# Optimization experiments

Hardware: AMD Instinct MI355X
Metric: run time of the kernel (lower is better)

The kernel has to match this reference:

```python
import jax, jax.numpy as jnp
import numpy as np

K_CHEB = 3  # Chebyshev order K -> K+1 basis matrices, gcn order = K


def setup_inputs() -> dict:
    key = jax.random.key(0)
    ks = jax.random.split(key, 7)
    B, N, T, Cin, Cout, ndim = 32, 512, 12, 64, 64, 40
    support_len = K_CHEB + 1
    cin_total = (K_CHEB * support_len + 1) * Cin  # (order*support_len+1)*c_in = 832
    x = jax.random.normal(ks[0], (B, N, T, Cin), jnp.float32)
    adj = (jax.random.uniform(ks[1], (N, N)) < 0.05).astype(jnp.float32)
    adjacency = jnp.maximum(adj, jnp.eye(N, dtype=jnp.float32))
    embedding = jax.random.uniform(ks[2], (N, ndim), dtype=jnp.float32)  # nn.init.uniform_
    W1 = jax.random.normal(ks[3], (ndim, ndim // 2), jnp.float32) * 0.3
    W2 = jax.random.normal(ks[4], (ndim, ndim // 2), jnp.float32) * 0.3
    mlp_w = jax.random.normal(ks[5], (Cout, cin_total), jnp.float32) / np.float32(np.sqrt(cin_total))
    mlp_b = jnp.zeros((Cout,), jnp.float32)
    return {"x": x, "adjacency": adjacency, "embedding": embedding,
            "W1": W1, "W2": W2, "mlp_w": mlp_w, "mlp_b": mlp_b}


def _cheb_kernels(adjacency, embedding, W1, W2):
    # adaptive adjacency: embedding mixed through column-softmaxed projections
    e1 = embedding @ jax.nn.softmax(W1, axis=0)
    e2 = embedding @ jax.nn.softmax(W2, axis=0)
    e1 = e1 / (jnp.linalg.norm(e1, axis=1, keepdims=True) + 1e-8)
    e2 = e2 / (jnp.linalg.norm(e2, axis=1, keepdims=True) + 1e-8)
    weight = e1 @ e2.T  # (N, N)
    A = jnp.where(adjacency > 0.0, weight + adjacency, jnp.asarray(9e-15, adjacency.dtype))
    # symmetric normalization: L = I - D^-1/2 A D^-1/2 ; Ls = (2/maxeig)*L - I with maxeig=2 -> Ls = -sym(A)
    d = 1.0 / jnp.sqrt(A.sum(axis=1))
    Ls = -(d[:, None] * A * d[None, :])
    I = jnp.eye(A.shape[0], dtype=A.dtype)
    kernels = [I, Ls]
    for _ in range(1, K_CHEB):  # Chebyshev recursion: T_{k+1} = 2 Ls T_k - T_{k-1}
        kernels.append(2.0 * (Ls @ kernels[-1]) - kernels[-2])
    return kernels  # K_CHEB + 1 matrices of (N, N)


def reference(x, adjacency, embedding, W1, W2, mlp_w, mlp_b):
    supports = _cheb_kernels(adjacency, embedding, W1, W2)
    xp = jnp.transpose(x, (0, 3, 1, 2))  # (B, Cin, N, T)
    out = [xp]
    for a in supports:
        x1 = jnp.einsum('bcvt,vw->bcwt', xp, a)
        out.append(x1)
        for _ in range(2, K_CHEB + 1):  # gcn order = K_CHEB
            x1 = jnp.einsum('bcvt,vw->bcwt', x1, a)
            out.append(x1)
    h = jnp.concatenate(out, axis=1)  # (B, 832, N, T)
    h = jnp.einsum('bcvt,oc->bovt', h, mlp_w) + mlp_b[None, :, None, None]  # 1x1 conv
    h = jnp.transpose(h, (0, 2, 3, 1))  # (B, N, T, Cout)
    return jax.nn.relu(h + x)  # conv_r is None (Cin == Cout), dropout eval no-op
```

## Files before the change

kernel.cpp:

```cpp
#include <hip/hip_runtime.h>
#include <hip/hip_bf16.h>

typedef unsigned short ushortT;
typedef unsigned int uintT;
typedef __attribute__((ext_vector_type(8))) short bf16x8;
typedef __attribute__((ext_vector_type(4))) float f32x4;
typedef __attribute__((ext_vector_type(4))) unsigned short us4;

__device__ __forceinline__ ushortT f2bf(float f) {
    union { float f; uintT u; } x; x.f = f;
    uintT r = x.u + 0x7fffu + ((x.u >> 16) & 1u);
    return (ushortT)(r >> 16);
}
__device__ __forceinline__ float bf2f(ushortT u) {
    union { uintT u; float f; } x; x.u = ((uintT)u) << 16; return x.f;
}

__global__ __launch_bounds__(256) void k_embed(const float* __restrict__ emb,
                                               const float* __restrict__ W1,
                                               const float* __restrict__ W2,
                                               float* __restrict__ e1,
                                               float* __restrict__ e2) {
    __shared__ float sW[800];
    __shared__ float sWs[800];
    const float* W = (blockIdx.x == 0) ? W1 : W2;
    float* e = (blockIdx.x == 0) ? e1 : e2;
    int tid = threadIdx.x;
    for (int i = tid; i < 800; i += 256) sW[i] = W[i];
    __syncthreads();
    if (tid < 20) {
        float mx = -1e30f;
        for (int i = 0; i < 40; ++i) mx = fmaxf(mx, sW[i * 20 + tid]);
        float s = 0.f;
        for (int i = 0; i < 40; ++i) s += __expf(sW[i * 20 + tid] - mx);
        float inv = 1.f / s;
        for (int i = 0; i < 40; ++i) sWs[i * 20 + tid] = __expf(sW[i * 20 + tid] - mx) * inv;
    }
    __syncthreads();
    for (int row = tid; row < 512; row += 256) {
        float acc[20];
        #pragma unroll
        for (int j = 0; j < 20; ++j) acc[j] = 0.f;
        for (int i = 0; i < 40; ++i) {
            float ev = emb[row * 40 + i];
            #pragma unroll
            for (int j = 0; j < 20; ++j) acc[j] += ev * sWs[i * 20 + j];
        }
        float s = 0.f;
        #pragma unroll
        for (int j = 0; j < 20; ++j) s += acc[j] * acc[j];
        float scale = 1.f / (sqrtf(s) + 1e-8f);
        #pragma unroll
        for (int j = 0; j < 20; ++j) e[row * 20 + j] = acc[j] * scale;
    }
}

__global__ __launch_bounds__(256) void k_adj(const float* __restrict__ adj,
                                             const float* __restrict__ e1,
                                             const float* __restrict__ e2,
                                             float* __restrict__ A,
                                             float* __restrict__ d) {
    int v = blockIdx.x, tid = threadIdx.x;
    __shared__ float ev[20];
    if (tid < 20) ev[tid] = e1[v * 20 + tid];
    __syncthreads();
    float local = 0.f;
    for (int w = tid; w < 512; w += 256) {
        float dot = 0.f;
        #pragma unroll
        for (int j = 0; j < 20; ++j) dot += ev[j] * e2[w * 20 + j];
        float av = adj[v * 512 + w];
        float Av = (av > 0.f) ? (dot + av) : 9e-15f;
        A[v * 512 + w] = Av;
        local += Av;
    }
    __shared__ float red[256];
    red[tid] = local;
    __syncthreads();
    for (int s = 128; s > 0; s >>= 1) {
        if (tid < s) red[tid] += red[tid + s];
        __syncthreads();
    }
    if (tid == 0) d[v] = 1.f / sqrtf(red[0]);
}

__global__ __launch_bounds__(256) void k_m(const float* __restrict__ A,
                                           const float* __restrict__ d,
                                           ushortT* __restrict__ P) {
    int w = blockIdx.x, tid = threadIdx.x;
    float dw = d[w];
    for (int v = tid; v < 512; v += 256) {
        float val = -d[v] * dw * A[v * 512 + w];
        P[512 * 512 + w * 512 + v] = f2bf(val);
    }
}

__global__ __launch_bounds__(256) void k_w(const float* __restrict__ mlp_w,
                                           ushortT* __restrict__ Wq) {
    int idx = blockIdx.x * 256 + threadIdx.x;
    if (idx >= 10 * 64 * 64) return;
    int q = idx >> 12, rem = idx & 4095, o = rem >> 6, c = rem & 63;
    float v;
    if (q == 0) {
        v = 0.f;
        #pragma unroll
        for (int k = 0; k < 4; ++k) v += mlp_w[o * 832 + k * 64 + c];
    } else {
        v = mlp_w[o * 832 + (q + 3) * 64 + c];
    }
    Wq[idx] = f2bf(v);
}

__global__ __launch_bounds__(256) void k_xbf(const float* __restrict__ x,
                                             ushortT* __restrict__ xbf) {
    size_t i = (size_t)blockIdx.x * 256 + threadIdx.x;
    int c = (int)(i & 15) * 4;
    int v = (int)((i >> 4) & 511);
    int bt = (int)(i >> 13);
    int b = bt / 12, t = bt - b * 12;
    f32x4 f = *(const f32x4*)(x + (((size_t)b * 512 + v) * 12 + t) * 64 + c);
    us4 o = { f2bf(f[0]), f2bf(f[1]), f2bf(f[2]), f2bf(f[3]) };
    *(us4*)(xbf + ((size_t)bt * 512 + v) * 64 + c) = o;
}

__global__ __launch_bounds__(256) void k_gemm512(const ushortT* __restrict__ A,
                                                 const ushortT* __restrict__ B,
                                                 ushortT* __restrict__ out1,
                                                 ushortT* __restrict__ out2,
                                                 int mode,
                                                 const ushortT* __restrict__ aux,
                                                 const ushortT* __restrict__ A2,
                                                 const ushortT* __restrict__ B2,
                                                 ushortT* __restrict__ out3) {
    int bx = blockIdx.x;
    if (bx >= 64) { A = A2; B = B2; out1 = out3; out2 = nullptr; mode = 0; bx -= 64; }
    int wave = threadIdx.x >> 6, lane = threadIdx.x & 63;
    int lr = lane & 15, lg = lane >> 4;
    int mbase = (bx >> 3) * 64;
    int nbase = (bx & 7) * 64 + wave * 16;
    f32x4 acc[4] = {};
    for (int kk = 0; kk < 16; ++kk) {
        int k0 = kk * 32 + lg * 8;
        bf16x8 bfr;
        #pragma unroll
        for (int j = 0; j < 8; ++j) bfr[j] = (short)B[(k0 + j) * 512 + nbase + lr];
        #pragma unroll
        for (int wt = 0; wt < 4; ++wt) {
            bf16x8 af = *(const bf16x8*)(A + (mbase + wt * 16 + lr) * 512 + k0);
            acc[wt] = __builtin_amdgcn_mfma_f32_16x16x32_bf16(af, bfr, acc[wt], 0, 0, 0);
        }
    }
    #pragma unroll
    for (int wt = 0; wt < 4; ++wt)
        #pragma unroll
        for (int r = 0; r < 4; ++r) {
            int row = mbase + wt * 16 + lg * 4 + r;
            int col = nbase + lr;
            float v = acc[wt][r];
            out1[row * 512 + col] = f2bf(v);
            if (mode == 1) out2[row * 512 + col] = f2bf(2.f * v - (row == col ? 1.f : 0.f));
            else if (mode == 2) out2[row * 512 + col] = f2bf(4.f * v - 3.f * bf2f(aux[row * 512 + col]));
        }
}

template<bool XBF>
__global__ __launch_bounds__(512, 4) void k_main(const float* __restrict__ x,
                                                 const ushortT* __restrict__ xbf,
                                                 const ushortT* __restrict__ P,
                                                 const ushortT* __restrict__ Wq,
                                                 const float* __restrict__ bias,
                                                 float* __restrict__ out) {
    __shared__ ushortT Zt[64 * 512];
    const int SZ = 512 * 512;
    int bid = blockIdx.x;
    int b = bid / 24, rr = bid % 24, tt = rr >> 1, half = rr & 1;
    int tid = threadIdx.x, wave = tid >> 6, lane = tid & 63;
    int lr = lane & 15, lg = lane >> 4;
    int wbase = half * 256 + wave * 32;
    int vbase = wave * 64;
    int mk = (lr & 7) << 3;

    const ushortT* xq = xbf + ((size_t)(b * 12 + tt) * 512 + vbase) * 64;
    const float*   xqf = x + ((size_t)(b * 512 + vbase) * 12 + tt) * 64;

    f32x4 oacc[2][4] = {};
    bf16x8 a0r[2], a1r[2];
    {
        const ushortT* pq1 = P + (size_t)SZ + (size_t)(wbase + lr) * 512 + lg * 8;
        a0r[0] = *(const bf16x8*)(pq1);
        a0r[1] = *(const bf16x8*)(pq1 + 32);
        a1r[0] = *(const bf16x8*)(pq1 + 8192);
        a1r[1] = *(const bf16x8*)(pq1 + 8192 + 32);
    }

    for (int q = 0; q <= 9; ++q) {
        bf16x8 xf[8];
        #pragma unroll
        for (int vt = 0; vt < 4; ++vt) {
            if (XBF) {
                xf[vt * 2 + 0] = *(const bf16x8*)(xq + (vt * 16 + lr) * 64 + lg * 8);
                xf[vt * 2 + 1] = *(const bf16x8*)(xq + (vt * 16 + lr) * 64 + 32 + lg * 8);
            } else {
                const float* px = xqf + (size_t)(vt * 16 + lr) * 768 + lg * 8;
                f32x4 f0 = *(const f32x4*)px;
                f32x4 f1 = *(const f32x4*)(px + 4);
                f32x4 f2 = *(const f32x4*)(px + 32);
                f32x4 f3 = *(const f32x4*)(px + 36);
                bf16x8 v0, v1;
                v0[0] = (short)f2bf(f0[0]); v0[1] = (short)f2bf(f0[1]);
                v0[2] = (short)f2bf(f0[2]); v0[3] = (short)f2bf(f0[3]);
                v0[4] = (short)f2bf(f1[0]); v0[5] = (short)f2bf(f1[1]);
                v0[6] = (short)f2bf(f1[2]); v0[7] = (short)f2bf(f1[3]);
                v1[0] = (short)f2bf(f2[0]); v1[1] = (short)f2bf(f2[1]);
                v1[2] = (short)f2bf(f2[2]); v1[3] = (short)f2bf(f2[3]);
                v1[4] = (short)f2bf(f3[0]); v1[5] = (short)f2bf(f3[1]);
                v1[6] = (short)f2bf(f3[2]); v1[7] = (short)f2bf(f3[3]);
                xf[vt * 2 + 0] = v0;
                xf[vt * 2 + 1] = v1;
            }
        }
        const ushortT* wqp = Wq + q * 4096;
        #pragma unroll
        for (int ot = 0; ot < 4; ++ot) {
            int o = ot * 16 + lr;
            bf16x8 wf0 = *(const bf16x8*)(wqp + o * 64 + lg * 8);
            bf16x8 wf1 = *(const bf16x8*)(wqp + o * 64 + 32 + lg * 8);
            f32x4 z0 = {}, z1 = {}, z2 = {}, z3 = {};
            z0 = __builtin_amdgcn_mfma_f32_16x16x32_bf16(xf[0], wf0, z0, 0, 0, 0);
            z0 = __builtin_amdgcn_mfma_f32_16x16x32_bf16(xf[1], wf1, z0, 0, 0, 0);
            z1 = __builtin_amdgcn_mfma_f32_16x16x32_bf16(xf[2], wf0, z1, 0, 0, 0);
            z1 = __builtin_amdgcn_mfma_f32_16x16x32_bf16(xf[3], wf1, z1, 0, 0, 0);
            z2 = __builtin_amdgcn_mfma_f32_16x16x32_bf16(xf[4], wf0, z2, 0, 0, 0);
            z2 = __builtin_amdgcn_mfma_f32_16x16x32_bf16(xf[5], wf1, z2, 0, 0, 0);
            z3 = __builtin_amdgcn_mfma_f32_16x16x32_bf16(xf[6], wf0, z3, 0, 0, 0);
            z3 = __builtin_amdgcn_mfma_f32_16x16x32_bf16(xf[7], wf1, z3, 0, 0, 0);
            int zb = o * 512;
            {
                int v0i = vbase + 0 * 16 + lg * 4;
                us4 pk = { f2bf(z0[0]), f2bf(z0[1]), f2bf(z0[2]), f2bf(z0[3]) };
                *(us4*)&Zt[zb + (v0i ^ mk)] = pk;
            }
            {
                int v0i = vbase + 1 * 16 + lg * 4;
                us4 pk = { f2bf(z1[0]), f2bf(z1[1]), f2bf(z1[2]), f2bf(z1[3]) };
                *(us4*)&Zt[zb + (v0i ^ mk)] = pk;
            }
            {
                int v0i = vbase + 2 * 16 + lg * 4;
                us4 pk = { f2bf(z2[0]), f2bf(z2[1]), f2bf(z2[2]), f2bf(z2[3]) };
                *(us4*)&Zt[zb + (v0i ^ mk)] = pk;
            }
            {
                int v0i = vbase + 3 * 16 + lg * 4;
                us4 pk = { f2bf(z3[0]), f2bf(z3[1]), f2bf(z3[2]), f2bf(z3[3]) };
                *(us4*)&Zt[zb + (v0i ^ mk)] = pk;
            }
        }
        __syncthreads();

        if (q == 0) {
            #pragma unroll
            for (int wt = 0; wt < 2; ++wt)
                #pragma unroll
                for (int ot = 0; ot < 4; ++ot) {
                    int o = ot * 16 + lr;
                    int w0 = wbase + wt * 16 + lg * 4;
                    us4 z4 = *(const us4*)&Zt[o * 512 + (w0 ^ mk)];
                    oacc[wt][ot][0] = bf2f(z4[0]);
                    oacc[wt][ot][1] = bf2f(z4[1]);
                    oacc[wt][ot][2] = bf2f(z4[2]);
                    oacc[wt][ot][3] = bf2f(z4[3]);
                }
        } else {
            const ushortT* pq  = P + (size_t)q * SZ + (size_t)(wbase + lr) * 512 + lg * 8;
            const ushortT* pqn = pq + SZ;
            #pragma unroll
            for (int kk = 0; kk < 16; ++kk) {
                const int slot = kk & 1;
                int vb = (kk * 32 + lg * 8) ^ mk;
                bf16x8 b0 = *(const bf16x8*)&Zt[(0 * 16 + lr) * 512 + vb];
                bf16x8 b1 = *(const bf16x8*)&Zt[(1 * 16 + lr) * 512 + vb];
                bf16x8 b2 = *(const bf16x8*)&Zt[(2 * 16 + lr) * 512 + vb];
                bf16x8 b3 = *(const bf16x8*)&Zt[(3 * 16 + lr) * 512 + vb];
                oacc[0][0] = __builtin_amdgcn_mfma_f32_16x16x32_bf16(a0r[slot], b0, oacc[0][0], 0, 0, 0);
                oacc[1][0] = __builtin_amdgcn_mfma_f32_16x16x32_bf16(a1r[slot], b0, oacc[1][0], 0, 0, 0);
                oacc[0][1] = __builtin_amdgcn_mfma_f32_16x16x32_bf16(a0r[slot], b1, oacc[0][1], 0, 0, 0);
                oacc[1][1] = __builtin_amdgcn_mfma_f32_16x16x32_bf16(a1r[slot], b1, oacc[1][1], 0, 0, 0);
                oacc[0][2] = __builtin_amdgcn_mfma_f32_16x16x32_bf16(a0r[slot], b2, oacc[0][2], 0, 0, 0);
                oacc[1][2] = __builtin_amdgcn_mfma_f32_16x16x32_bf16(a1r[slot], b2, oacc[1][2], 0, 0, 0);
                oacc[0][3] = __builtin_amdgcn_mfma_f32_16x16x32_bf16(a0r[slot], b3, oacc[0][3], 0, 0, 0);
                oacc[1][3] = __builtin_amdgcn_mfma_f32_16x16x32_bf16(a1r[slot], b3, oacc[1][3], 0, 0, 0);
                if (kk < 14) {
                    a0r[slot] = *(const bf16x8*)(pq + (kk + 2) * 32);
                    a1r[slot] = *(const bf16x8*)(pq + 8192 + (kk + 2) * 32);
                } else if (q < 9) {
                    a0r[slot] = *(const bf16x8*)(pqn + (kk - 14) * 32);
                    a1r[slot] = *(const bf16x8*)(pqn + 8192 + (kk - 14) * 32);
                }
            }
        }
        __syncthreads();
    }

    #pragma unroll
    for (int wt = 0; wt < 2; ++wt)
        #pragma unroll
        for (int ot = 0; ot < 4; ++ot)
            #pragma unroll
            for (int r = 0; r < 4; ++r) {
                int w = wbase + wt * 16 + lg * 4 + r;
                int o = ot * 16 + lr;
                size_t oi = (((size_t)b * 512 + w) * 12 + tt) * 64 + o;
                float v = oacc[wt][ot][r] + x[oi] + bias[o];
                out[oi] = (v > 0.f) ? v : 0.f;
            }
}

extern "C" void kernel_launch(void* const* d_in, const int* in_sizes, int n_in,
                              void* d_out, int out_size, void* d_ws, size_t ws_size,
                              hipStream_t stream) {
    const float* x    = (const float*)d_in[0];
    const float* adj  = (const float*)d_in[1];
    const float* emb  = (const float*)d_in[2];
    const float* W1   = (const float*)d_in[3];
    const float* W2   = (const float*)d_in[4];
    const float* mlpw = (const float*)d_in[5];
    const float* mlpb = (const float*)d_in[6];
    float* out = (float*)d_out;

    char* ws = (char*)d_ws;
    float*   e1   = (float*)(ws + 0);
    float*   e2   = (float*)(ws + 65536);
    float*   A    = (float*)(ws + 131072);
    float*   dvec = (float*)(ws + 1179648);
    ushortT* P    = (ushortT*)(ws + 1183744);
    ushortT* Wq   = (ushortT*)(ws + 6426624);
    ushortT* xbf  = (ushortT*)(ws + 6508544);
    const size_t WS_NEED = 6508544 + (size_t)32 * 12 * 512 * 64 * 2;
    const bool use_xbf = (ws_size >= WS_NEED);

    k_embed<<<2, 256, 0, stream>>>(emb, W1, W2, e1, e2);
    k_adj<<<512, 256, 0, stream>>>(adj, e1, e2, A, dvec);
    k_m<<<512, 256, 0, stream>>>(A, dvec, P);
    k_w<<<160, 256, 0, stream>>>(mlpw, Wq);
    if (use_xbf) k_xbf<<<12288, 256, 0, stream>>>(x, xbf);

    const int SZ = 512 * 512;
    ushortT *S1 = P + 1 * SZ, *S2 = P + 2 * SZ, *S3 = P + 3 * SZ, *S4 = P + 4 * SZ,
            *S5 = P + 5 * SZ, *S6 = P + 6 * SZ, *S7 = P + 7 * SZ, *S8 = P + 8 * SZ,
            *S9 = P + 9 * SZ;
    k_gemm512<<<64, 256, 0, stream>>>(S1, S1, S2, S4, 1, nullptr, nullptr, nullptr, nullptr);
    k_gemm512<<<64, 256, 0, stream>>>(S1, S2, S3, S7, 2, S1, nullptr, nullptr, nullptr);
    k_gemm512<<<128, 256, 0, stream>>>(S4, S4, S5, nullptr, 0, nullptr, S7, S7, S8);
    k_gemm512<<<128, 256, 0, stream>>>(S4, S5, S6, nullptr, 0, nullptr, S7, S8, S9);

    if (use_xbf)
        k_main<true><<<768, 512, 0, stream>>>(x, xbf, P, Wq, mlpb, out);
    else
        k_main<false><<<768, 512, 0, stream>>>(x, nullptr, P, Wq, mlpb, out);
    (void)in_sizes; (void)n_in; (void)out_size;
}
```

Measured before the change: 374.9 us.

## Pad LDS tile, deepen A-prefetch, fuse prep kernels, rebalance support GEMM chain

Replaces the XOR-swizzled Zt shared-memory layout with a padded row stride of 520 to avoid bank conflicts. The main kernel now prefetches A fragments four k-steps ahead instead of two, and splits the projection stage into two halves to lower register pressure. The Wq and bf16-x conversion kernels are merged into a single launch, and the Chebyshev support GEMMs are re-paired so each launch runs two independent products. The padding makes the Zt array larger, and the deeper prefetch needs more registers, which could reduce occupancy.

```diff
diff --git a/kernel.cpp b/kernel.cpp
--- a/kernel.cpp
+++ b/kernel.cpp
@@ -15,6 +15,8 @@
 __device__ __forceinline__ float bf2f(ushortT u) {
     union { uintT u; float f; } x; x.u = ((uintT)u) << 16; return x.f;
 }
+
+#define ZLD 520
 
 __global__ __launch_bounds__(256) void k_embed(const float* __restrict__ emb,
                                                const float* __restrict__ W1,
@@ -95,32 +97,34 @@
     }
 }
 
-__global__ __launch_bounds__(256) void k_w(const float* __restrict__ mlp_w,
-                                           ushortT* __restrict__ Wq) {
-    int idx = blockIdx.x * 256 + threadIdx.x;
-    if (idx >= 10 * 64 * 64) return;
-    int q = idx >> 12, rem = idx & 4095, o = rem >> 6, c = rem & 63;
-    float v;
-    if (q == 0) {
-        v = 0.f;
-        #pragma unroll
-        for (int k = 0; k < 4; ++k) v += mlp_w[o * 832 + k * 64 + c];
+__global__ __launch_bounds__(256) void k_prep(const float* __restrict__ x,
+                                              ushortT* __restrict__ xbf,
+                                              const float* __restrict__ mlp_w,
+                                              ushortT* __restrict__ Wq) {
+    int bx = blockIdx.x;
+    if (bx < 160) {
+        int idx = bx * 256 + threadIdx.x;
+        if (idx >= 10 * 64 * 64) return;
+        int q = idx >> 12, rem = idx & 4095, o = rem >> 6, c = rem & 63;
+        float v;
+        if (q == 0) {
+            v = 0.f;
+            #pragma unroll
+            for (int k = 0; k < 4; ++k) v += mlp_w[o * 832 + k * 64 + c];
+        } else {
+            v = mlp_w[o * 832 + (q + 3) * 64 + c];
+        }
+        Wq[idx] = f2bf(v);
     } else {
-        v = mlp_w[o * 832 + (q + 3) * 64 + c];
-    }
-    Wq[idx] = f2bf(v);
-}
-
-__global__ __launch_bounds__(256) void k_xbf(const float* __restrict__ x,
-                                             ushortT* __restrict__ xbf) {
-    size_t i = (size_t)blockIdx.x * 256 + threadIdx.x;
-    int c = (int)(i & 15) * 4;
-    int v = (int)((i >> 4) & 511);
-    int bt = (int)(i >> 13);
-    int b = bt / 12, t = bt - b * 12;
-    f32x4 f = *(const f32x4*)(x + (((size_t)b * 512 + v) * 12 + t) * 64 + c);
-    us4 o = { f2bf(f[0]), f2bf(f[1]), f2bf(f[2]), f2bf(f[3]) };
-    *(us4*)(xbf + ((size_t)bt * 512 + v) * 64 + c) = o;
+        size_t i = (size_t)(bx - 160) * 256 + threadIdx.x;
+        int c = (int)(i & 15) * 4;
+        int v = (int)((i >> 4) & 511);
+        int bt = (int)(i >> 13);
+        int b = bt / 12, t = bt - b * 12;
+        f32x4 f = *(const f32x4*)(x + (((size_t)b * 512 + v) * 12 + t) * 64 + c);
+        us4 o = { f2bf(f[0]), f2bf(f[1]), f2bf(f[2]), f2bf(f[3]) };
+        *(us4*)(xbf + ((size_t)bt * 512 + v) * 64 + c) = o;
+    }
 }
 
 __global__ __launch_bounds__(256) void k_gemm512(const ushortT* __restrict__ A,
@@ -170,7 +174,7 @@
                                                  const ushortT* __restrict__ Wq,
                                                  const float* __restrict__ bias,
                                                  float* __restrict__ out) {
-    __shared__ ushortT Zt[64 * 512];
+    __shared__ ushortT Zt[64 * ZLD];
     const int SZ = 512 * 512;
     int bid = blockIdx.x;
     int b = bid / 24, rr = bid % 24, tt = rr >> 1, half = rr & 1;
@@ -178,82 +182,72 @@
     int lr = lane & 15, lg = lane >> 4;
     int wbase = half * 256 + wave * 32;
     int vbase = wave * 64;
-    int mk = (lr & 7) << 3;
 
     const ushortT* xq = xbf + ((size_t)(b * 12 + tt) * 512 + vbase) * 64;
     const float*   xqf = x + ((size_t)(b * 512 + vbase) * 12 + tt) * 64;
 
     f32x4 oacc[2][4] = {};
-    bf16x8 a0r[2], a1r[2];
+    bf16x8 a0r[4], a1r[4];
     {
         const ushortT* pq1 = P + (size_t)SZ + (size_t)(wbase + lr) * 512 + lg * 8;
-        a0r[0] = *(const bf16x8*)(pq1);
-        a0r[1] = *(const bf16x8*)(pq1 + 32);
-        a1r[0] = *(const bf16x8*)(pq1 + 8192);
-        a1r[1] = *(const bf16x8*)(pq1 + 8192 + 32);
+        #pragma unroll
+        for (int s = 0; s < 4; ++s) {
+            a0r[s] = *(const bf16x8*)(pq1 + s * 32);
+            a1r[s] = *(const bf16x8*)(pq1 + 8192 + s * 32);
+        }
     }
 
     for (int q = 0; q <= 9; ++q) {
-        bf16x8 xf[8];
-        #pragma unroll
-        for (int vt = 0; vt < 4; ++vt) {
-            if (XBF) {
-                xf[vt * 2 + 0] = *(const bf16x8*)(xq + (vt * 16 + lr) * 64 + lg * 8);
-                xf[vt * 2 + 1] = *(const bf16x8*)(xq + (vt * 16 + lr) * 64 + 32 + lg * 8);
-            } else {
-                const float* px = xqf + (size_t)(vt * 16 + lr) * 768 + lg * 8;
-                f32x4 f0 = *(const f32x4*)px;
-                f32x4 f1 = *(const f32x4*)(px + 4);
-                f32x4 f2 = *(const f32x4*)(px + 32);
-                f32x4 f3 = *(const f32x4*)(px + 36);
-                bf16x8 v0, v1;
-                v0[0] = (short)f2bf(f0[0]); v0[1] = (short)f2bf(f0[1]);
-                v0[2] = (short)f2bf(f0[2]); v0[3] = (short)f2bf(f0[3]);
-                v0[4] = (short)f2bf(f1[0]); v0[5] = (short)f2bf(f1[1]);
-                v0[6] = (short)f2bf(f1[2]); v0[7] = (short)f2bf(f1[3]);
-                v1[0] = (short)f2bf(f2[0]); v1[1] = (short)f2bf(f2[1]);
-                v1[2] = (short)f2bf(f2[2]); v1[3] = (short)f2bf(f2[3]);
-                v1[4] = (short)f2bf(f3[0]); v1[5] = (short)f2bf(f3[1]);
-                v1[6] = (short)f2bf(f3[2]); v1[7] = (short)f2bf(f3[3]);
-                xf[vt * 2 + 0] = v0;
-                xf[vt * 2 + 1] = v1;
+        const ushortT* wqp = Wq + q * 4096;
+        #pragma unroll
+        for (int h = 0; h < 2; ++h) {
+            bf16x8 xf[4];
+            #pragma unroll
+            for (int j = 0; j < 2; ++j) {
+                int vrow = (h * 2 + j) * 16 + lr;
+                if (XBF) {
+                    xf[j * 2 + 0] = *(const bf16x8*)(xq + vrow * 64 + lg * 8);
+                    xf[j * 2 + 1] = *(const bf16x8*)(xq + vrow * 64 + 32 + lg * 8);
+                } else {
+                    const float* px = xqf + (size_t)vrow * 768 + lg * 8;
+                    f32x4 f0 = *(const f32x4*)px;
+                    f32x4 f1 = *(const f32x4*)(px + 4);
+                    f32x4 f2 = *(const f32x4*)(px + 32);
+                    f32x4 f3 = *(const f32x4*)(px + 36);
+                    bf16x8 v0, v1;
+                    v0[0] = (short)f2bf(f0[0]); v0[1] = (short)f2bf(f0[1]);
+                    v0[2] = (short)f2bf(f0[2]); v0[3] = (short)f2bf(f0[3]);
+                    v0[4] = (short)f2bf(f1[0]); v0[5] = (short)f2bf(f1[1]);
+                    v0[6] = (short)f2bf(f1[2]); v0[7] = (short)f2bf(f1[3]);
+                    v1[0] = (short)f2bf(f2[0]); v1[1] = (short)f2bf(f2[1]);
+                    v1[2] = (short)f2bf(f2[2]); v1[3] = (short)f2bf(f2[3]);
+                    v1[4] = (short)f2bf(f3[0]); v1[5] = (short)f2bf(f3[1]);
+                    v1[6] = (short)f2bf(f3[2]); v1[7] = (short)f2bf(f3[3]);
+                    xf[j * 2 + 0] = v0;
+                    xf[j * 2 + 1] = v1;
+                }
             }
-        }
-        const ushortT* wqp = Wq + q * 4096;
-        #pragma unroll
-        for (int ot = 0; ot < 4; ++ot) {
-            int o = ot * 16 + lr;
-            bf16x8 wf0 = *(const bf16x8*)(wqp + o * 64 + lg * 8);
-            bf16x8 wf1 = *(const bf16x8*)(wqp + o * 64 + 32 + lg * 8);
-            f32x4 z0 = {}, z1 = {}, z2 = {}, z3 = {};
-            z0 = __builtin_amdgcn_mfma_f32_16x16x32_bf16(xf[0], wf0, z0, 0, 0, 0);
-            z0 = __builtin_amdgcn_mfma_f32_16x16x32_bf16(xf[1], wf1, z0, 0, 0, 0);
-            z1 = __builtin_amdgcn_mfma_f32_16x16x32_bf16(xf[2], wf0, z1, 0, 0, 0);
-            z1 = __builtin_amdgcn_mfma_f32_16x16x32_bf16(xf[3], wf1, z1, 0, 0, 0);
-            z2 = __builtin_amdgcn_mfma_f32_16x16x32_bf16(xf[4], wf0, z2, 0, 0, 0);
-            z2 = __builtin_amdgcn_mfma_f32_16x16x32_bf16(xf[5], wf1, z2, 0, 0, 0);
-            z3 = __builtin_amdgcn_mfma_f32_16x16x32_bf16(xf[6], wf0, z3, 0, 0, 0);
-            z3 = __builtin_amdgcn_mfma_f32_16x16x32_bf16(xf[7], wf1, z3, 0, 0, 0);
-            int zb = o * 512;
-            {
-                int v0i = vbase + 0 * 16 + lg * 4;
-                us4 pk = { f2bf(z0[0]), f2bf(z0[1]), f2bf(z0[2]), f2bf(z0[3]) };
-                *(us4*)&Zt[zb + (v0i ^ mk)] = pk;
-            }
-            {
-                int v0i = vbase + 1 * 16 + lg * 4;
-                us4 pk = { f2bf(z1[0]), f2bf(z1[1]), f2bf(z1[2]), f2bf(z1[3]) };
-                *(us4*)&Zt[zb + (v0i ^ mk)] = pk;
-            }
-            {
-                int v0i = vbase + 2 * 16 + lg * 4;
-                us4 pk = { f2bf(z2[0]), f2bf(z2[1]), f2bf(z2[2]), f2bf(z2[3]) };
-                *(us4*)&Zt[zb + (v0i ^ mk)] = pk;
-            }
-            {
-                int v0i = vbase + 3 * 16 + lg * 4;
-                us4 pk = { f2bf(z3[0]), f2bf(z3[1]), f2bf(z3[2]), f2bf(z3[3]) };
-                *(us4*)&Zt[zb + (v0i ^ mk)] = pk;
+            #pragma unroll
+            for (int ot = 0; ot < 4; ++ot) {
+                int o = ot * 16 + lr;
+                bf16x8 wf0 = *(const bf16x8*)(wqp + o * 64 + lg * 8);
+                bf16x8 wf1 = *(const bf16x8*)(wqp + o * 64 + 32 + lg * 8);
+                f32x4 z0 = {}, z1 = {};
+                z0 = __builtin_amdgcn_mfma_f32_16x16x32_bf16(xf[0], wf0, z0, 0, 0, 0);
+                z0 = __builtin_amdgcn_mfma_f32_16x16x32_bf16(xf[1], wf1, z0, 0, 0, 0);
+                z1 = __builtin_amdgcn_mfma_f32_16x16x32_bf16(xf[2], wf0, z1, 0, 0, 0);
+                z1 = __builtin_amdgcn_mfma_f32_16x16x32_bf16(xf[3], wf1, z1, 0, 0, 0);
+                int zb = o * ZLD;
+                {
+                    int v0i = vbase + (h * 2 + 0) * 16 + lg * 4;
+                    us4 pk = { f2bf(z0[0]), f2bf(z0[1]), f2bf(z0[2]), f2bf(z0[3]) };
+                    *(us4*)&Zt[zb + v0i] = pk;
+                }
+                {
+                    int v0i = vbase + (h * 2 + 1) * 16 + lg * 4;
+                    us4 pk = { f2bf(z1[0]), f2bf(z1[1]), f2bf(z1[2]), f2bf(z1[3]) };
+                    *(us4*)&Zt[zb + v0i] = pk;
+                }
             }
         }
         __syncthreads();
@@ -265,7 +259,7 @@
                 for (int ot = 0; ot < 4; ++ot) {
                     int o = ot * 16 + lr;
                     int w0 = wbase + wt * 16 + lg * 4;
-                    us4 z4 = *(const us4*)&Zt[o * 512 + (w0 ^ mk)];
+                    us4 z4 = *(const us4*)&Zt[o * ZLD + w0];
                     oacc[wt][ot][0] = bf2f(z4[0]);
                     oacc[wt][ot][1] = bf2f(z4[1]);
                     oacc[wt][ot][2] = bf2f(z4[2]);
@@ -276,12 +270,12 @@
             const ushortT* pqn = pq + SZ;
             #pragma unroll
             for (int kk = 0; kk < 16; ++kk) {
-                const int slot = kk & 1;
-                int vb = (kk * 32 + lg * 8) ^ mk;
-                bf16x8 b0 = *(const bf16x8*)&Zt[(0 * 16 + lr) * 512 + vb];
-                bf16x8 b1 = *(const bf16x8*)&Zt[(1 * 16 + lr) * 512 + vb];
-                bf16x8 b2 = *(const bf16x8*)&Zt[(2 * 16 + lr) * 512 + vb];
-                bf16x8 b3 = *(const bf16x8*)&Zt[(3 * 16 + lr) * 512 + vb];
+                const int slot = kk & 3;
+                int vb = kk * 32 + lg * 8;
+                bf16x8 b0 = *(const bf16x8*)&Zt[(0 * 16 + lr) * ZLD + vb];
+                bf16x8 b1 = *(const bf16x8*)&Zt[(1 * 16 + lr) * ZLD + vb];
+                bf16x8 b2 = *(const bf16x8*)&Zt[(2 * 16 + lr) * ZLD + vb];
+                bf16x8 b3 = *(const bf16x8*)&Zt[(3 * 16 + lr) * ZLD + vb];
                 oacc[0][0] = __builtin_amdgcn_mfma_f32_16x16x32_bf16(a0r[slot], b0, oacc[0][0], 0, 0, 0);
                 oacc[1][0] = __builtin_amdgcn_mfma_f32_16x16x32_bf16(a1r[slot], b0, oacc[1][0], 0, 0, 0);
                 oacc[0][1] = __builtin_amdgcn_mfma_f32_16x16x32_bf16(a0r[slot], b1, oacc[0][1], 0, 0, 0);
@@ -290,12 +284,12 @@
                 oacc[1][2] = __builtin_amdgcn_mfma_f32_16x16x32_bf16(a1r[slot], b2, oacc[1][2], 0, 0, 0);
                 oacc[0][3] = __builtin_amdgcn_mfma_f32_16x16x32_bf16(a0r[slot], b3, oacc[0][3], 0, 0, 0);
                 oacc[1][3] = __builtin_amdgcn_mfma_f32_16x16x32_bf16(a1r[slot], b3, oacc[1][3], 0, 0, 0);
-                if (kk < 14) {
-                    a0r[slot] = *(const bf16x8*)(pq + (kk + 2) * 32);
-                    a1r[slot] = *(const bf16x8*)(pq + 8192 + (kk + 2) * 32);
+                if (kk < 12) {
+                    a0r[slot] = *(const bf16x8*)(pq + (kk + 4) * 32);
+                    a1r[slot] = *(const bf16x8*)(pq + 8192 + (kk + 4) * 32);
                 } else if (q < 9) {
-                    a0r[slot] = *(const bf16x8*)(pqn + (kk - 14) * 32);
-                    a1r[slot] = *(const bf16x8*)(pqn + 8192 + (kk - 14) * 32);
+                    a0r[slot] = *(const bf16x8*)(pqn + (kk - 12) * 32);
+                    a1r[slot] = *(const bf16x8*)(pqn + 8192 + (kk - 12) * 32);
                 }
             }
         }
@@ -342,17 +336,16 @@
     k_embed<<<2, 256, 0, stream>>>(emb, W1, W2, e1, e2);
     k_adj<<<512, 256, 0, stream>>>(adj, e1, e2, A, dvec);
     k_m<<<512, 256, 0, stream>>>(A, dvec, P);
-    k_w<<<160, 256, 0, stream>>>(mlpw, Wq);
-    if (use_xbf) k_xbf<<<12288, 256, 0, stream>>>(x, xbf);
+    k_prep<<<use_xbf ? 12448 : 160, 256, 0, stream>>>(x, xbf, mlpw, Wq);
 
     const int SZ = 512 * 512;
     ushortT *S1 = P + 1 * SZ, *S2 = P + 2 * SZ, *S3 = P + 3 * SZ, *S4 = P + 4 * SZ,
             *S5 = P + 5 * SZ, *S6 = P + 6 * SZ, *S7 = P + 7 * SZ, *S8 = P + 8 * SZ,
             *S9 = P + 9 * SZ;
     k_gemm512<<<64, 256, 0, stream>>>(S1, S1, S2, S4, 1, nullptr, nullptr, nullptr, nullptr);
-    k_gemm512<<<64, 256, 0, stream>>>(S1, S2, S3, S7, 2, S1, nullptr, nullptr, nullptr);
-    k_gemm512<<<128, 256, 0, stream>>>(S4, S4, S5, nullptr, 0, nullptr, S7, S7, S8);
-    k_gemm512<<<128, 256, 0, stream>>>(S4, S5, S6, nullptr, 0, nullptr, S7, S8, S9);
+    k_gemm512<<<128, 256, 0, stream>>>(S1, S2, S3, S7, 2, S1, S4, S4, S5);
+    k_gemm512<<<128, 256, 0, stream>>>(S4, S5, S6, nullptr, 0, nullptr, S7, S7, S8);
+    k_gemm512<<<64, 256, 0, stream>>>(S7, S8, S9, nullptr, 0, nullptr, nullptr, nullptr, nullptr);
 
     if (use_xbf)
         k_main<true><<<768, 512, 0, stream>>>(x, xbf, P, Wq, mlpb, out);
```

After: 472.4 us. 1.26x slower.
